# Kernel optimization log

Measured on AMD Instinct MI355X. Metric: run time of the kernel, lower is better.

Reference implementation:

```python
import jax, jax.numpy as jnp
import numpy as np

B = 65536
NUM_INPUTS = 256
NUM_HIDDEN = 256


def setup_inputs() -> dict:
    key = jax.random.key(0)
    ks = jax.random.split(key, 11)
    f32 = jnp.float32
    return {
        "x": jax.random.normal(ks[0], (B, NUM_INPUTS), dtype=f32),
        "h_t_1": jax.random.normal(ks[1], (B, NUM_HIDDEN), dtype=f32),
        "Wz": jax.random.normal(ks[2], (NUM_INPUTS, NUM_HIDDEN), dtype=f32),
        "Uz": jax.random.normal(ks[3], (NUM_HIDDEN, NUM_HIDDEN), dtype=f32),
        "bz": jax.random.normal(ks[4], (NUM_HIDDEN,), dtype=f32),
        "Wr": jax.random.normal(ks[5], (NUM_INPUTS, NUM_HIDDEN), dtype=f32),
        "Ur": jax.random.normal(ks[6], (NUM_HIDDEN, NUM_HIDDEN), dtype=f32),
        "br": jax.random.normal(ks[7], (NUM_HIDDEN,), dtype=f32),
        "Wh": jax.random.normal(ks[8], (NUM_INPUTS, NUM_HIDDEN), dtype=f32),
        "Uh": jax.random.normal(ks[9], (NUM_HIDDEN, NUM_HIDDEN), dtype=f32),
        "bh": jax.random.normal(ks[10], (NUM_HIDDEN,), dtype=f32),
    }


def reference(x, h_t_1, Wz, Uz, bz, Wr, Ur, br, Wh, Uh, bh):
    # update gate z = sigmoid(x@Wz + h@Uz + bz)
    z = jax.nn.sigmoid(x @ Wz + h_t_1 @ Uz + bz)
    # reset gate r = sigmoid(x@Wr + h@Ur + br)
    r = jax.nn.sigmoid(x @ Wr + h_t_1 @ Ur + br)
    # candidate: tanh(x@Wh + (r*h)@Uh + bh)
    h_hat = jnp.tanh(x @ Wh + (r * h_t_1) @ Uh + bh)
    h_t = z * h_t_1 + (1.0 - z) * h_hat
    return (h_t, h_t)
```

## Files before the change

### kernel.cpp

```cpp
#include <hip/hip_runtime.h>
#include <hip/hip_fp16.h>


#define NHID 256
#define B_ROWS 65536
#define MT 32
#define RT 2
#define CPW 4
#define GATE_STRIDE (16 * 16 * 64 * 8)

typedef _Float16 half8 __attribute__((ext_vector_type(8)));
typedef _Float16 half4_t __attribute__((ext_vector_type(4)));
typedef _Float16 half2_t __attribute__((ext_vector_type(2)));
typedef float floatx4 __attribute__((ext_vector_type(4)));

__device__ __forceinline__ int lidx(int m, int c) {
    return m * 256 + ((((c >> 3) ^ (m & 7)) << 3)) + (c & 7);
}

__device__ __forceinline__ void barrier_lgkm() {
    __builtin_amdgcn_sched_barrier(0);
    asm volatile("s_waitcnt lgkmcnt(0)" ::: "memory");
    __builtin_amdgcn_s_barrier();
    __builtin_amdgcn_sched_barrier(0);
}

__global__ __launch_bounds__(256) void pack_weights_kernel(
    const float* __restrict__ Wz, const float* __restrict__ Uz,
    const float* __restrict__ Wr, const float* __restrict__ Ur,
    const float* __restrict__ Wh, const float* __restrict__ Uh,
    _Float16* __restrict__ packed)
{
    int tid = blockIdx.x * blockDim.x + threadIdx.x;
    int lane = tid & 63;
    int s    = (tid >> 6) & 15;
    int ct   = (tid >> 10) & 15;
    int g    = tid >> 14;
    const float* W = (g == 0) ? Wz : (g == 1) ? Wr : Wh;
    const float* U = (g == 0) ? Uz : (g == 1) ? Ur : Uh;
    int n  = ct * 16 + (lane & 15);
    int k0 = s * 32 + (lane >> 4) * 8;
    half8 v;
#pragma unroll
    for (int j = 0; j < 8; ++j) {
        int k = k0 + j;
        float f = (k < 256) ? W[k * 256 + n] : U[(k - 256) * 256 + n];
        v[j] = (_Float16)f;
    }
    *reinterpret_cast<half8*>(packed + (size_t)tid * 8) = v;
}

#define WFRAG(base, ct, s) \
    (*reinterpret_cast<const half8*>((base) + (size_t)((((ct) * 16 + (s)) * 64 + lane) * 8)))

__global__ __launch_bounds__(256, 2) void gru_main_kernel(
    const float* __restrict__ x, const float* __restrict__ h,
    const _Float16* __restrict__ wpack,
    const float* __restrict__ bz, const float* __restrict__ br,
    const float* __restrict__ bh,
    float* __restrict__ out)
{
    __shared__ __align__(16) _Float16 lsm[MT * 256 * 2];
    _Float16* lx = lsm;
    _Float16* lh = lsm + MT * 256;

    const int tid  = threadIdx.x;
    const int lane = tid & 63;
    const int wave = tid >> 6;
    const int row0 = blockIdx.x * MT;
    const int m_lo = lane & 15;
    const int quad = lane >> 4;
    const int mx   = m_lo & 7;
    const int ct0  = wave * CPW;

    const _Float16* wz = wpack;
    const _Float16* wr = wpack + GATE_STRIDE;
    const _Float16* wh = wpack + 2 * GATE_STRIDE;

    half8 wzb[2][2], wrb[2][2];
    wzb[0][0] = WFRAG(wz, ct0 + 0, 0);
    wzb[0][1] = WFRAG(wz, ct0 + 1, 0);
    wrb[0][0] = WFRAG(wr, ct0 + 0, 0);
    wrb[0][1] = WFRAG(wr, ct0 + 1, 0);

    {
        const float4* xv = reinterpret_cast<const float4*>(x + (size_t)row0 * NHID);
        const float4* hv = reinterpret_cast<const float4*>(h + (size_t)row0 * NHID);
#pragma unroll
        for (int it = 0; it < (MT * 64) / 256; ++it) {
            int i = it * 256 + tid;
            int m = i >> 6;
            int c = (i & 63) * 4;
            float4 a = xv[i];
            float4 b = hv[i];
            half4_t va = { (_Float16)a.x, (_Float16)a.y, (_Float16)a.z, (_Float16)a.w };
            half4_t vb = { (_Float16)b.x, (_Float16)b.y, (_Float16)b.z, (_Float16)b.w };
            *reinterpret_cast<half4_t*>(&lx[lidx(m, c)]) = va;
            *reinterpret_cast<half4_t*>(&lh[lidx(m, c)]) = vb;
        }
    }
    barrier_lgkm();

    half2_t zpk[CPW][RT][4];

    floatx4 accz[CPW][RT];
    floatx4 accr[CPW][RT];
#pragma unroll
    for (int c = 0; c < CPW; ++c)
#pragma unroll
        for (int rt = 0; rt < RT; ++rt) {
            accz[c][rt] = (floatx4){0.f, 0.f, 0.f, 0.f};
            accr[c][rt] = (floatx4){0.f, 0.f, 0.f, 0.f};
        }

#pragma unroll
    for (int s = 0; s < 16; ++s) {
        const _Float16* asrc = (s < 8) ? lx : lh;
        const int kcx = (((s & 7) * 4 + quad) ^ mx) << 3;
        half8 af[RT];
#pragma unroll
        for (int rt = 0; rt < RT; ++rt)
            af[rt] = *reinterpret_cast<const half8*>(&asrc[(rt * 16 + m_lo) * 256 + kcx]);
#pragma unroll
        for (int p = 0; p < 2; ++p) {
            const int u = s * 2 + p;
            if (u < 31) {
                const int ns = (p == 1) ? s + 1 : s;
                const int nc = ct0 + (p ^ 1) * 2;
                wzb[p ^ 1][0] = WFRAG(wz, nc + 0, ns);
                wzb[p ^ 1][1] = WFRAG(wz, nc + 1, ns);
                wrb[p ^ 1][0] = WFRAG(wr, nc + 0, ns);
                wrb[p ^ 1][1] = WFRAG(wr, nc + 1, ns);
            }
            __builtin_amdgcn_s_setprio(1);
#pragma unroll
            for (int q = 0; q < 2; ++q) {
                const int c = p * 2 + q;
#pragma unroll
                for (int rt = 0; rt < RT; ++rt) {
                    accz[c][rt] = __builtin_amdgcn_mfma_f32_16x16x32_f16(af[rt], wzb[p][q], accz[c][rt], 0, 0, 0);
                    accr[c][rt] = __builtin_amdgcn_mfma_f32_16x16x32_f16(af[rt], wrb[p][q], accr[c][rt], 0, 0, 0);
                }
            }
            __builtin_amdgcn_s_setprio(0);
        }
    }

    half8 whb[2][2];
    whb[0][0] = WFRAG(wh, ct0 + 0, 0);
    whb[0][1] = WFRAG(wh, ct0 + 1, 0);
    float bzv[CPW], brv[CPW], bhv[CPW];
#pragma unroll
    for (int c = 0; c < CPW; ++c) {
        const int col = (ct0 + c) * 16 + m_lo;
        bzv[c] = bz[col];
        brv[c] = br[col];
        bhv[c] = bh[col];
    }

    barrier_lgkm();

#pragma unroll
    for (int c = 0; c < CPW; ++c) {
        const int col = (ct0 + c) * 16 + m_lo;
#pragma unroll
        for (int rt = 0; rt < RT; ++rt) {
#pragma unroll
            for (int e = 0; e < 4; ++e) {
                const int row = rt * 16 + quad * 4 + e;
                float sz = accz[c][rt][e] + bzv[c];
                float sr = accr[c][rt][e] + brv[c];
                float zv = 1.f / (1.f + __expf(-sz));
                float rv = 1.f / (1.f + __expf(-sr));
                const int li = lidx(row, col);
                float hval = (float)lh[li];
                lh[li] = (_Float16)(rv * hval);
                zpk[c][rt][e] = half2_t{ (_Float16)(zv * hval), (_Float16)(1.f - zv) };
            }
        }
    }

    floatx4 acch[CPW][RT];
#pragma unroll
    for (int c = 0; c < CPW; ++c)
#pragma unroll
        for (int rt = 0; rt < RT; ++rt)
            acch[c][rt] = (floatx4){0.f, 0.f, 0.f, 0.f};

#pragma unroll
    for (int s = 0; s < 16; ++s) {
        if (s == 8) barrier_lgkm();
        const _Float16* asrc = (s < 8) ? lx : lh;
        const int kcx = (((s & 7) * 4 + quad) ^ mx) << 3;
        half8 af[RT];
#pragma unroll
        for (int rt = 0; rt < RT; ++rt)
            af[rt] = *reinterpret_cast<const half8*>(&asrc[(rt * 16 + m_lo) * 256 + kcx]);
#pragma unroll
        for (int p = 0; p < 2; ++p) {
            const int u = s * 2 + p;
            if (u < 31) {
                const int ns = (p == 1) ? s + 1 : s;
                const int nc = ct0 + (p ^ 1) * 2;
                whb[p ^ 1][0] = WFRAG(wh, nc + 0, ns);
                whb[p ^ 1][1] = WFRAG(wh, nc + 1, ns);
            }
            __builtin_amdgcn_s_setprio(1);
#pragma unroll
            for (int q = 0; q < 2; ++q) {
                const int c = p * 2 + q;
#pragma unroll
                for (int rt = 0; rt < RT; ++rt)
                    acch[c][rt] = __builtin_amdgcn_mfma_f32_16x16x32_f16(af[rt], whb[p][q], acch[c][rt], 0, 0, 0);
            }
            __builtin_amdgcn_s_setprio(0);
        }
    }

    const size_t OUT2 = (size_t)B_ROWS * NHID;
#pragma unroll
    for (int c = 0; c < CPW; ++c) {
        const int col = (ct0 + c) * 16 + m_lo;
#pragma unroll
        for (int rt = 0; rt < RT; ++rt) {
#pragma unroll
            for (int e = 0; e < 4; ++e) {
                const int row = rt * 16 + quad * 4 + e;
                float sh = acch[c][rt][e] + bhv[c];
                float e2 = __expf(2.f * sh);
                float hh = 1.f - 2.f / (e2 + 1.f);
                float zh  = (float)zpk[c][rt][e][0];
                float omz = (float)zpk[c][rt][e][1];
                float ht  = zh + omz * hh;
                size_t idx = (size_t)(row0 + row) * NHID + col;
                __builtin_nontemporal_store(ht, &out[idx]);
                __builtin_nontemporal_store(ht, &out[OUT2 + idx]);
            }
        }
    }
}

extern "C" void kernel_launch(void* const* d_in, const int* in_sizes, int n_in,
                              void* d_out, int out_size, void* d_ws, size_t ws_size,
                              hipStream_t stream) {
    (void)in_sizes; (void)n_in; (void)out_size; (void)ws_size;
    const float* x  = (const float*)d_in[0];
    const float* h  = (const float*)d_in[1];
    const float* Wz = (const float*)d_in[2];
    const float* Uz = (const float*)d_in[3];
    const float* bz = (const float*)d_in[4];
    const float* Wr = (const float*)d_in[5];
    const float* Ur = (const float*)d_in[6];
    const float* br = (const float*)d_in[7];
    const float* Wh = (const float*)d_in[8];
    const float* Uh = (const float*)d_in[9];
    const float* bh = (const float*)d_in[10];
    float* out = (float*)d_out;
    _Float16* wpack = (_Float16*)d_ws;

    pack_weights_kernel<<<192, 256, 0, stream>>>(Wz, Uz, Wr, Ur, Wh, Uh, wpack);
    gru_main_kernel<<<B_ROWS / MT, 256, 0, stream>>>(x, h, wpack, bz, br, bh, out);
}
```

Measured before the change: 312.4 us.

## Process two row tiles per block with next-tile input prefetch overlapped

```diff
diff --git a/kernel.cpp b/kernel.cpp
--- a/kernel.cpp
+++ b/kernel.cpp
@@ -7,6 +7,7 @@
 #define MT 32
 #define RT 2
 #define CPW 4
+#define NBLK 1024
 #define GATE_STRIDE (16 * 16 * 64 * 8)
 
 typedef _Float16 half8 __attribute__((ext_vector_type(8)));
@@ -67,88 +68,24 @@
     const int tid  = threadIdx.x;
     const int lane = tid & 63;
     const int wave = tid >> 6;
-    const int row0 = blockIdx.x * MT;
     const int m_lo = lane & 15;
     const int quad = lane >> 4;
     const int mx   = m_lo & 7;
     const int ct0  = wave * CPW;
+    const int sc   = (tid & 63) * 4;
 
     const _Float16* wz = wpack;
     const _Float16* wr = wpack + GATE_STRIDE;
     const _Float16* wh = wpack + 2 * GATE_STRIDE;
-
-    half8 wzb[2][2], wrb[2][2];
-    wzb[0][0] = WFRAG(wz, ct0 + 0, 0);
-    wzb[0][1] = WFRAG(wz, ct0 + 1, 0);
-    wrb[0][0] = WFRAG(wr, ct0 + 0, 0);
-    wrb[0][1] = WFRAG(wr, ct0 + 1, 0);
-
-    {
-        const float4* xv = reinterpret_cast<const float4*>(x + (size_t)row0 * NHID);
-        const float4* hv = reinterpret_cast<const float4*>(h + (size_t)row0 * NHID);
-#pragma unroll
-        for (int it = 0; it < (MT * 64) / 256; ++it) {
-            int i = it * 256 + tid;
-            int m = i >> 6;
-            int c = (i & 63) * 4;
-            float4 a = xv[i];
-            float4 b = hv[i];
-            half4_t va = { (_Float16)a.x, (_Float16)a.y, (_Float16)a.z, (_Float16)a.w };
-            half4_t vb = { (_Float16)b.x, (_Float16)b.y, (_Float16)b.z, (_Float16)b.w };
-            *reinterpret_cast<half4_t*>(&lx[lidx(m, c)]) = va;
-            *reinterpret_cast<half4_t*>(&lh[lidx(m, c)]) = vb;
-        }
-    }
-    barrier_lgkm();
-
-    half2_t zpk[CPW][RT][4];
-
-    floatx4 accz[CPW][RT];
-    floatx4 accr[CPW][RT];
-#pragma unroll
-    for (int c = 0; c < CPW; ++c)
-#pragma unroll
-        for (int rt = 0; rt < RT; ++rt) {
-            accz[c][rt] = (floatx4){0.f, 0.f, 0.f, 0.f};
-            accr[c][rt] = (floatx4){0.f, 0.f, 0.f, 0.f};
-        }
-
-#pragma unroll
-    for (int s = 0; s < 16; ++s) {
-        const _Float16* asrc = (s < 8) ? lx : lh;
-        const int kcx = (((s & 7) * 4 + quad) ^ mx) << 3;
-        half8 af[RT];
-#pragma unroll
-        for (int rt = 0; rt < RT; ++rt)
-            af[rt] = *reinterpret_cast<const half8*>(&asrc[(rt * 16 + m_lo) * 256 + kcx]);
-#pragma unroll
-        for (int p = 0; p < 2; ++p) {
-            const int u = s * 2 + p;
-            if (u < 31) {
-                const int ns = (p == 1) ? s + 1 : s;
-                const int nc = ct0 + (p ^ 1) * 2;
-                wzb[p ^ 1][0] = WFRAG(wz, nc + 0, ns);
-                wzb[p ^ 1][1] = WFRAG(wz, nc + 1, ns);
-                wrb[p ^ 1][0] = WFRAG(wr, nc + 0, ns);
-                wrb[p ^ 1][1] = WFRAG(wr, nc + 1, ns);
-            }
-            __builtin_amdgcn_s_setprio(1);
-#pragma unroll
-            for (int q = 0; q < 2; ++q) {
-                const int c = p * 2 + q;
-#pragma unroll
-                for (int rt = 0; rt < RT; ++rt) {
-                    accz[c][rt] = __builtin_amdgcn_mfma_f32_16x16x32_f16(af[rt], wzb[p][q], accz[c][rt], 0, 0, 0);
-                    accr[c][rt] = __builtin_amdgcn_mfma_f32_16x16x32_f16(af[rt], wrb[p][q], accr[c][rt], 0, 0, 0);
-                }
-            }
-            __builtin_amdgcn_s_setprio(0);
-        }
-    }
-
-    half8 whb[2][2];
-    whb[0][0] = WFRAG(wh, ct0 + 0, 0);
-    whb[0][1] = WFRAG(wh, ct0 + 1, 0);
+    const float4* xv4 = reinterpret_cast<const float4*>(x);
+    const float4* hv4 = reinterpret_cast<const float4*>(h);
+
+    auto stage_wr = [&](_Float16* dst, const float4& v, int it) {
+        const int m = it * 4 + wave;
+        half4_t p = { (_Float16)v.x, (_Float16)v.y, (_Float16)v.z, (_Float16)v.w };
+        *reinterpret_cast<half4_t*>(&dst[lidx(m, sc)]) = p;
+    };
+
     float bzv[CPW], brv[CPW], bhv[CPW];
 #pragma unroll
     for (int c = 0; c < CPW; ++c) {
@@ -158,84 +95,193 @@
         bhv[c] = bh[col];
     }
 
+    half8 wzb[2][2], wrb[2][2];
+    wzb[0][0] = WFRAG(wz, ct0 + 0, 0);
+    wzb[0][1] = WFRAG(wz, ct0 + 1, 0);
+    wrb[0][0] = WFRAG(wr, ct0 + 0, 0);
+    wrb[0][1] = WFRAG(wr, ct0 + 1, 0);
+
+    {
+        const size_t ib = (size_t)(blockIdx.x * MT) * 64 + tid;
+#pragma unroll
+        for (int it = 0; it < 8; ++it) {
+            float4 a = xv4[ib + it * 256];
+            float4 b = hv4[ib + it * 256];
+            stage_wr(lx, a, it);
+            stage_wr(lh, b, it);
+        }
+    }
     barrier_lgkm();
 
-#pragma unroll
-    for (int c = 0; c < CPW; ++c) {
-        const int col = (ct0 + c) * 16 + m_lo;
-#pragma unroll
-        for (int rt = 0; rt < RT; ++rt) {
-#pragma unroll
-            for (int e = 0; e < 4; ++e) {
-                const int row = rt * 16 + quad * 4 + e;
-                float sz = accz[c][rt][e] + bzv[c];
-                float sr = accr[c][rt][e] + brv[c];
-                float zv = 1.f / (1.f + __expf(-sz));
-                float rv = 1.f / (1.f + __expf(-sr));
-                const int li = lidx(row, col);
-                float hval = (float)lh[li];
-                lh[li] = (_Float16)(rv * hval);
-                zpk[c][rt][e] = half2_t{ (_Float16)(zv * hval), (_Float16)(1.f - zv) };
-            }
-        }
-    }
-
-    floatx4 acch[CPW][RT];
-#pragma unroll
-    for (int c = 0; c < CPW; ++c)
-#pragma unroll
-        for (int rt = 0; rt < RT; ++rt)
-            acch[c][rt] = (floatx4){0.f, 0.f, 0.f, 0.f};
-
-#pragma unroll
-    for (int s = 0; s < 16; ++s) {
-        if (s == 8) barrier_lgkm();
-        const _Float16* asrc = (s < 8) ? lx : lh;
-        const int kcx = (((s & 7) * 4 + quad) ^ mx) << 3;
-        half8 af[RT];
-#pragma unroll
-        for (int rt = 0; rt < RT; ++rt)
-            af[rt] = *reinterpret_cast<const half8*>(&asrc[(rt * 16 + m_lo) * 256 + kcx]);
-#pragma unroll
-        for (int p = 0; p < 2; ++p) {
-            const int u = s * 2 + p;
-            if (u < 31) {
-                const int ns = (p == 1) ? s + 1 : s;
-                const int nc = ct0 + (p ^ 1) * 2;
-                whb[p ^ 1][0] = WFRAG(wh, nc + 0, ns);
-                whb[p ^ 1][1] = WFRAG(wh, nc + 1, ns);
-            }
-            __builtin_amdgcn_s_setprio(1);
-#pragma unroll
-            for (int q = 0; q < 2; ++q) {
-                const int c = p * 2 + q;
-#pragma unroll
-                for (int rt = 0; rt < RT; ++rt)
-                    acch[c][rt] = __builtin_amdgcn_mfma_f32_16x16x32_f16(af[rt], whb[p][q], acch[c][rt], 0, 0, 0);
-            }
-            __builtin_amdgcn_s_setprio(0);
-        }
-    }
-
     const size_t OUT2 = (size_t)B_ROWS * NHID;
-#pragma unroll
-    for (int c = 0; c < CPW; ++c) {
-        const int col = (ct0 + c) * 16 + m_lo;
-#pragma unroll
-        for (int rt = 0; rt < RT; ++rt) {
-#pragma unroll
-            for (int e = 0; e < 4; ++e) {
-                const int row = rt * 16 + quad * 4 + e;
-                float sh = acch[c][rt][e] + bhv[c];
-                float e2 = __expf(2.f * sh);
-                float hh = 1.f - 2.f / (e2 + 1.f);
-                float zh  = (float)zpk[c][rt][e][0];
-                float omz = (float)zpk[c][rt][e][1];
-                float ht  = zh + omz * hh;
-                size_t idx = (size_t)(row0 + row) * NHID + col;
-                __builtin_nontemporal_store(ht, &out[idx]);
-                __builtin_nontemporal_store(ht, &out[OUT2 + idx]);
-            }
+
+#pragma unroll
+    for (int tile = 0; tile < 2; ++tile) {
+        const int row0   = (blockIdx.x + tile * NBLK) * MT;
+        const size_t nib = (size_t)((blockIdx.x + NBLK) * MT) * 64 + tid;
+
+        half2_t zpk[CPW][RT][4];
+
+        floatx4 accz[CPW][RT];
+        floatx4 accr[CPW][RT];
+#pragma unroll
+        for (int c = 0; c < CPW; ++c)
+#pragma unroll
+            for (int rt = 0; rt < RT; ++rt) {
+                accz[c][rt] = (floatx4){0.f, 0.f, 0.f, 0.f};
+                accr[c][rt] = (floatx4){0.f, 0.f, 0.f, 0.f};
+            }
+
+#pragma unroll
+        for (int s = 0; s < 16; ++s) {
+            if (tile == 1 && s == 8) barrier_lgkm();
+            const _Float16* asrc = (s < 8) ? lx : lh;
+            const int kcx = (((s & 7) * 4 + quad) ^ mx) << 3;
+            half8 af[RT];
+#pragma unroll
+            for (int rt = 0; rt < RT; ++rt)
+                af[rt] = *reinterpret_cast<const half8*>(&asrc[(rt * 16 + m_lo) * 256 + kcx]);
+#pragma unroll
+            for (int p = 0; p < 2; ++p) {
+                const int u = s * 2 + p;
+                if (u < 31) {
+                    const int ns = (p == 1) ? s + 1 : s;
+                    const int nc = ct0 + (p ^ 1) * 2;
+                    wzb[p ^ 1][0] = WFRAG(wz, nc + 0, ns);
+                    wzb[p ^ 1][1] = WFRAG(wz, nc + 1, ns);
+                    wrb[p ^ 1][0] = WFRAG(wr, nc + 0, ns);
+                    wrb[p ^ 1][1] = WFRAG(wr, nc + 1, ns);
+                }
+                __builtin_amdgcn_s_setprio(1);
+#pragma unroll
+                for (int q = 0; q < 2; ++q) {
+                    const int c = p * 2 + q;
+#pragma unroll
+                    for (int rt = 0; rt < RT; ++rt) {
+                        accz[c][rt] = __builtin_amdgcn_mfma_f32_16x16x32_f16(af[rt], wzb[p][q], accz[c][rt], 0, 0, 0);
+                        accr[c][rt] = __builtin_amdgcn_mfma_f32_16x16x32_f16(af[rt], wrb[p][q], accr[c][rt], 0, 0, 0);
+                    }
+                }
+                __builtin_amdgcn_s_setprio(0);
+            }
+        }
+
+        half8 whb[2][2];
+        whb[0][0] = WFRAG(wh, ct0 + 0, 0);
+        whb[0][1] = WFRAG(wh, ct0 + 1, 0);
+
+        barrier_lgkm();
+
+#pragma unroll
+        for (int c = 0; c < CPW; ++c) {
+#pragma unroll
+            for (int rt = 0; rt < RT; ++rt) {
+#pragma unroll
+                for (int e = 0; e < 4; ++e) {
+                    const int row = rt * 16 + quad * 4 + e;
+                    const int col = (ct0 + c) * 16 + m_lo;
+                    float sz = accz[c][rt][e] + bzv[c];
+                    float sr = accr[c][rt][e] + brv[c];
+                    float zv = 1.f / (1.f + __expf(-sz));
+                    float rv = 1.f / (1.f + __expf(-sr));
+                    const int li = lidx(row, col);
+                    float hval = (float)lh[li];
+                    lh[li] = (_Float16)(rv * hval);
+                    zpk[c][rt][e] = half2_t{ (_Float16)(zv * hval), (_Float16)(1.f - zv) };
+                }
+            }
+        }
+
+        floatx4 acch[CPW][RT];
+#pragma unroll
+        for (int c = 0; c < CPW; ++c)
+#pragma unroll
+            for (int rt = 0; rt < RT; ++rt)
+                acch[c][rt] = (floatx4){0.f, 0.f, 0.f, 0.f};
+
+        float4 xra[4], xrb[4], hr[8];
+
+#pragma unroll
+        for (int s = 0; s < 16; ++s) {
+            if (s == 8) {
+                barrier_lgkm();
+                if (tile == 0) {
+#pragma unroll
+                    for (int it = 0; it < 4; ++it)
+                        xra[it] = xv4[nib + it * 256];
+                }
+            }
+            if (s == 12 && tile == 0) {
+#pragma unroll
+                for (int it = 0; it < 4; ++it) stage_wr(lx, xra[it], it);
+#pragma unroll
+                for (int it = 0; it < 4; ++it)
+                    xrb[it] = xv4[nib + (it + 4) * 256];
+            }
+            const _Float16* asrc = (s < 8) ? lx : lh;
+            const int kcx = (((s & 7) * 4 + quad) ^ mx) << 3;
+            half8 af[RT];
+#pragma unroll
+            for (int rt = 0; rt < RT; ++rt)
+                af[rt] = *reinterpret_cast<const half8*>(&asrc[(rt * 16 + m_lo) * 256 + kcx]);
+#pragma unroll
+            for (int p = 0; p < 2; ++p) {
+                const int u = s * 2 + p;
+                if (u < 31) {
+                    const int ns = (p == 1) ? s + 1 : s;
+                    const int nc = ct0 + (p ^ 1) * 2;
+                    whb[p ^ 1][0] = WFRAG(wh, nc + 0, ns);
+                    whb[p ^ 1][1] = WFRAG(wh, nc + 1, ns);
+                }
+                __builtin_amdgcn_s_setprio(1);
+#pragma unroll
+                for (int q = 0; q < 2; ++q) {
+                    const int c = p * 2 + q;
+#pragma unroll
+                    for (int rt = 0; rt < RT; ++rt)
+                        acch[c][rt] = __builtin_amdgcn_mfma_f32_16x16x32_f16(af[rt], whb[p][q], acch[c][rt], 0, 0, 0);
+                }
+                __builtin_amdgcn_s_setprio(0);
+            }
+        }
+
+        if (tile == 0) {
+#pragma unroll
+            for (int it = 0; it < 4; ++it) stage_wr(lx, xrb[it], it + 4);
+#pragma unroll
+            for (int it = 0; it < 8; ++it) hr[it] = hv4[nib + it * 256];
+            wzb[0][0] = WFRAG(wz, ct0 + 0, 0);
+            wzb[0][1] = WFRAG(wz, ct0 + 1, 0);
+            wrb[0][0] = WFRAG(wr, ct0 + 0, 0);
+            wrb[0][1] = WFRAG(wr, ct0 + 1, 0);
+        }
+
+        barrier_lgkm();
+
+#pragma unroll
+        for (int c = 0; c < CPW; ++c) {
+            const int col = (ct0 + c) * 16 + m_lo;
+#pragma unroll
+            for (int rt = 0; rt < RT; ++rt) {
+#pragma unroll
+                for (int e = 0; e < 4; ++e) {
+                    const int row = rt * 16 + quad * 4 + e;
+                    float sh = acch[c][rt][e] + bhv[c];
+                    float e2 = __expf(2.f * sh);
+                    float hh = 1.f - 2.f / (e2 + 1.f);
+                    float zh  = (float)zpk[c][rt][e][0];
+                    float omz = (float)zpk[c][rt][e][1];
+                    float ht  = zh + omz * hh;
+                    size_t idx = (size_t)(row0 + row) * NHID + col;
+                    out[idx] = ht;
+                    out[OUT2 + idx] = ht;
+                }
+            }
+        }
+
+        if (tile == 0) {
+#pragma unroll
+            for (int it = 0; it < 8; ++it) stage_wr(lh, hr[it], it);
         }
     }
 }
@@ -259,5 +305,5 @@
     _Float16* wpack = (_Float16*)d_ws;
 
     pack_weights_kernel<<<192, 256, 0, stream>>>(Wz, Uz, Wr, Ur, Wh, Uh, wpack);
-    gru_main_kernel<<<B_ROWS / MT, 256, 0, stream>>>(x, h, wpack, bz, br, bh, out);
-}
+    gru_main_kernel<<<NBLK, 256, 0, stream>>>(x, h, wpack, bz, br, bh, out);
+}
```

Result: no change. 314.4 us (+0.6%).

## Make blocks loop over four row tiles with double-buffered LDS prefetch

Applied to the files above, without the earlier changes.

```diff
diff --git a/kernel.cpp b/kernel.cpp
--- a/kernel.cpp
+++ b/kernel.cpp
@@ -7,6 +7,9 @@
 #define MT 32
 #define RT 2
 #define CPW 4
+#define TPB 4
+#define NBLK 512
+#define TILEH (MT * 256)
 #define GATE_STRIDE (16 * 16 * 64 * 8)
 
 typedef _Float16 half8 __attribute__((ext_vector_type(8)));
@@ -60,22 +63,38 @@
     const float* __restrict__ bh,
     float* __restrict__ out)
 {
-    __shared__ __align__(16) _Float16 lsm[MT * 256 * 2];
-    _Float16* lx = lsm;
-    _Float16* lh = lsm + MT * 256;
-
-    const int tid  = threadIdx.x;
-    const int lane = tid & 63;
-    const int wave = tid >> 6;
-    const int row0 = blockIdx.x * MT;
-    const int m_lo = lane & 15;
-    const int quad = lane >> 4;
-    const int mx   = m_lo & 7;
-    const int ct0  = wave * CPW;
+    __shared__ __align__(16) _Float16 lsm[4 * TILEH];
+
+    const int tid   = threadIdx.x;
+    const int lane  = tid & 63;
+    const int wave  = tid >> 6;
+    const int m_lo  = lane & 15;
+    const int quad  = lane >> 4;
+    const int mx    = m_lo & 7;
+    const int ct0   = wave * CPW;
+    const int lane4 = lane * 4;
 
     const _Float16* wz = wpack;
     const _Float16* wr = wpack + GATE_STRIDE;
     const _Float16* wh = wpack + 2 * GATE_STRIDE;
+    const float4* xv4 = reinterpret_cast<const float4*>(x);
+    const float4* hv4 = reinterpret_cast<const float4*>(h);
+    const size_t OUT2 = (size_t)B_ROWS * NHID;
+
+    auto stage_wr = [&](_Float16* dst, const float4& v, int j) {
+        const int m = j * 4 + wave;
+        half4_t p = { (_Float16)v.x, (_Float16)v.y, (_Float16)v.z, (_Float16)v.w };
+        *reinterpret_cast<half4_t*>(&dst[lidx(m, lane4)]) = p;
+    };
+
+    float bzv[CPW], brv[CPW], bhv[CPW];
+#pragma unroll
+    for (int c = 0; c < CPW; ++c) {
+        const int col = (ct0 + c) * 16 + m_lo;
+        bzv[c] = bz[col];
+        brv[c] = br[col];
+        bhv[c] = bh[col];
+    }
 
     half8 wzb[2][2], wrb[2][2];
     wzb[0][0] = WFRAG(wz, ct0 + 0, 0);
@@ -84,157 +103,171 @@
     wrb[0][1] = WFRAG(wr, ct0 + 1, 0);
 
     {
-        const float4* xv = reinterpret_cast<const float4*>(x + (size_t)row0 * NHID);
-        const float4* hv = reinterpret_cast<const float4*>(h + (size_t)row0 * NHID);
-#pragma unroll
-        for (int it = 0; it < (MT * 64) / 256; ++it) {
-            int i = it * 256 + tid;
-            int m = i >> 6;
-            int c = (i & 63) * 4;
-            float4 a = xv[i];
-            float4 b = hv[i];
-            half4_t va = { (_Float16)a.x, (_Float16)a.y, (_Float16)a.z, (_Float16)a.w };
-            half4_t vb = { (_Float16)b.x, (_Float16)b.y, (_Float16)b.z, (_Float16)b.w };
-            *reinterpret_cast<half4_t*>(&lx[lidx(m, c)]) = va;
-            *reinterpret_cast<half4_t*>(&lh[lidx(m, c)]) = vb;
+        const size_t ib = (size_t)(blockIdx.x * TPB * MT) * 64 + tid;
+#pragma unroll
+        for (int j = 0; j < 8; ++j) {
+            float4 a = xv4[ib + j * 256];
+            float4 b = hv4[ib + j * 256];
+            stage_wr(lsm, a, j);
+            stage_wr(lsm + TILEH, b, j);
         }
     }
     barrier_lgkm();
 
-    half2_t zpk[CPW][RT][4];
-
-    floatx4 accz[CPW][RT];
-    floatx4 accr[CPW][RT];
-#pragma unroll
-    for (int c = 0; c < CPW; ++c)
-#pragma unroll
-        for (int rt = 0; rt < RT; ++rt) {
-            accz[c][rt] = (floatx4){0.f, 0.f, 0.f, 0.f};
-            accr[c][rt] = (floatx4){0.f, 0.f, 0.f, 0.f};
-        }
-
-#pragma unroll
-    for (int s = 0; s < 16; ++s) {
-        const _Float16* asrc = (s < 8) ? lx : lh;
-        const int kcx = (((s & 7) * 4 + quad) ^ mx) << 3;
-        half8 af[RT];
-#pragma unroll
-        for (int rt = 0; rt < RT; ++rt)
-            af[rt] = *reinterpret_cast<const half8*>(&asrc[(rt * 16 + m_lo) * 256 + kcx]);
-#pragma unroll
-        for (int p = 0; p < 2; ++p) {
-            const int u = s * 2 + p;
-            if (u < 31) {
-                const int ns = (p == 1) ? s + 1 : s;
-                const int nc = ct0 + (p ^ 1) * 2;
-                wzb[p ^ 1][0] = WFRAG(wz, nc + 0, ns);
-                wzb[p ^ 1][1] = WFRAG(wz, nc + 1, ns);
-                wrb[p ^ 1][0] = WFRAG(wr, nc + 0, ns);
-                wrb[p ^ 1][1] = WFRAG(wr, nc + 1, ns);
-            }
-            __builtin_amdgcn_s_setprio(1);
-#pragma unroll
-            for (int q = 0; q < 2; ++q) {
-                const int c = p * 2 + q;
-#pragma unroll
-                for (int rt = 0; rt < RT; ++rt) {
-                    accz[c][rt] = __builtin_amdgcn_mfma_f32_16x16x32_f16(af[rt], wzb[p][q], accz[c][rt], 0, 0, 0);
-                    accr[c][rt] = __builtin_amdgcn_mfma_f32_16x16x32_f16(af[rt], wrb[p][q], accr[c][rt], 0, 0, 0);
-                }
-            }
-            __builtin_amdgcn_s_setprio(0);
-        }
-    }
-
-    half8 whb[2][2];
-    whb[0][0] = WFRAG(wh, ct0 + 0, 0);
-    whb[0][1] = WFRAG(wh, ct0 + 1, 0);
-    float bzv[CPW], brv[CPW], bhv[CPW];
-#pragma unroll
-    for (int c = 0; c < CPW; ++c) {
-        const int col = (ct0 + c) * 16 + m_lo;
-        bzv[c] = bz[col];
-        brv[c] = br[col];
-        bhv[c] = bh[col];
-    }
-
-    barrier_lgkm();
-
-#pragma unroll
-    for (int c = 0; c < CPW; ++c) {
-        const int col = (ct0 + c) * 16 + m_lo;
-#pragma unroll
-        for (int rt = 0; rt < RT; ++rt) {
-#pragma unroll
-            for (int e = 0; e < 4; ++e) {
-                const int row = rt * 16 + quad * 4 + e;
-                float sz = accz[c][rt][e] + bzv[c];
-                float sr = accr[c][rt][e] + brv[c];
-                float zv = 1.f / (1.f + __expf(-sz));
-                float rv = 1.f / (1.f + __expf(-sr));
-                const int li = lidx(row, col);
-                float hval = (float)lh[li];
-                lh[li] = (_Float16)(rv * hval);
-                zpk[c][rt][e] = half2_t{ (_Float16)(zv * hval), (_Float16)(1.f - zv) };
-            }
-        }
-    }
-
-    floatx4 acch[CPW][RT];
-#pragma unroll
-    for (int c = 0; c < CPW; ++c)
-#pragma unroll
-        for (int rt = 0; rt < RT; ++rt)
-            acch[c][rt] = (floatx4){0.f, 0.f, 0.f, 0.f};
-
-#pragma unroll
-    for (int s = 0; s < 16; ++s) {
-        if (s == 8) barrier_lgkm();
-        const _Float16* asrc = (s < 8) ? lx : lh;
-        const int kcx = (((s & 7) * 4 + quad) ^ mx) << 3;
-        half8 af[RT];
-#pragma unroll
-        for (int rt = 0; rt < RT; ++rt)
-            af[rt] = *reinterpret_cast<const half8*>(&asrc[(rt * 16 + m_lo) * 256 + kcx]);
-#pragma unroll
-        for (int p = 0; p < 2; ++p) {
-            const int u = s * 2 + p;
-            if (u < 31) {
-                const int ns = (p == 1) ? s + 1 : s;
-                const int nc = ct0 + (p ^ 1) * 2;
-                whb[p ^ 1][0] = WFRAG(wh, nc + 0, ns);
-                whb[p ^ 1][1] = WFRAG(wh, nc + 1, ns);
-            }
-            __builtin_amdgcn_s_setprio(1);
-#pragma unroll
-            for (int q = 0; q < 2; ++q) {
-                const int c = p * 2 + q;
-#pragma unroll
-                for (int rt = 0; rt < RT; ++rt)
-                    acch[c][rt] = __builtin_amdgcn_mfma_f32_16x16x32_f16(af[rt], whb[p][q], acch[c][rt], 0, 0, 0);
-            }
-            __builtin_amdgcn_s_setprio(0);
-        }
-    }
-
-    const size_t OUT2 = (size_t)B_ROWS * NHID;
-#pragma unroll
-    for (int c = 0; c < CPW; ++c) {
-        const int col = (ct0 + c) * 16 + m_lo;
-#pragma unroll
-        for (int rt = 0; rt < RT; ++rt) {
-#pragma unroll
-            for (int e = 0; e < 4; ++e) {
-                const int row = rt * 16 + quad * 4 + e;
-                float sh = acch[c][rt][e] + bhv[c];
-                float e2 = __expf(2.f * sh);
-                float hh = 1.f - 2.f / (e2 + 1.f);
-                float zh  = (float)zpk[c][rt][e][0];
-                float omz = (float)zpk[c][rt][e][1];
-                float ht  = zh + omz * hh;
-                size_t idx = (size_t)(row0 + row) * NHID + col;
-                __builtin_nontemporal_store(ht, &out[idx]);
-                __builtin_nontemporal_store(ht, &out[OUT2 + idx]);
+#pragma unroll 1
+    for (int t = 0; t < TPB; ++t) {
+        const int buf = t & 1;
+        _Float16* lxc = lsm + buf * (2 * TILEH);
+        _Float16* lhc = lxc + TILEH;
+        _Float16* lxn = lsm + (buf ^ 1) * (2 * TILEH);
+        _Float16* lhn = lxn + TILEH;
+        const int row0 = (blockIdx.x * TPB + t) * MT;
+        const size_t nib = (size_t)(row0 + MT) * 64 + tid;
+        const bool more = (t < TPB - 1);
+
+        half2_t zpk[CPW][RT][4];
+
+        floatx4 accz[CPW][RT];
+        floatx4 accr[CPW][RT];
+#pragma unroll
+        for (int c = 0; c < CPW; ++c)
+#pragma unroll
+            for (int rt = 0; rt < RT; ++rt) {
+                accz[c][rt] = (floatx4){0.f, 0.f, 0.f, 0.f};
+                accr[c][rt] = (floatx4){0.f, 0.f, 0.f, 0.f};
+            }
+
+        float4 xin;
+#pragma unroll
+        for (int s = 0; s < 16; ++s) {
+            if (more) {
+                if ((s & 1) == 0) xin = xv4[nib + (s >> 1) * 256];
+                else              stage_wr(lxn, xin, s >> 1);
+            }
+            const _Float16* asrc = (s < 8) ? lxc : lhc;
+            const int kcx = (((s & 7) * 4 + quad) ^ mx) << 3;
+            half8 af[RT];
+#pragma unroll
+            for (int rt = 0; rt < RT; ++rt)
+                af[rt] = *reinterpret_cast<const half8*>(&asrc[(rt * 16 + m_lo) * 256 + kcx]);
+#pragma unroll
+            for (int p = 0; p < 2; ++p) {
+                const int u = s * 2 + p;
+                if (u < 31) {
+                    const int ns = (p == 1) ? s + 1 : s;
+                    const int nc = ct0 + (p ^ 1) * 2;
+                    wzb[p ^ 1][0] = WFRAG(wz, nc + 0, ns);
+                    wzb[p ^ 1][1] = WFRAG(wz, nc + 1, ns);
+                    wrb[p ^ 1][0] = WFRAG(wr, nc + 0, ns);
+                    wrb[p ^ 1][1] = WFRAG(wr, nc + 1, ns);
+                }
+                __builtin_amdgcn_s_setprio(1);
+#pragma unroll
+                for (int q = 0; q < 2; ++q) {
+                    const int c = p * 2 + q;
+#pragma unroll
+                    for (int rt = 0; rt < RT; ++rt) {
+                        accz[c][rt] = __builtin_amdgcn_mfma_f32_16x16x32_f16(af[rt], wzb[p][q], accz[c][rt], 0, 0, 0);
+                        accr[c][rt] = __builtin_amdgcn_mfma_f32_16x16x32_f16(af[rt], wrb[p][q], accr[c][rt], 0, 0, 0);
+                    }
+                }
+                __builtin_amdgcn_s_setprio(0);
+            }
+        }
+
+        half8 whb[2][2];
+        whb[0][0] = WFRAG(wh, ct0 + 0, 0);
+        whb[0][1] = WFRAG(wh, ct0 + 1, 0);
+
+        barrier_lgkm();
+
+#pragma unroll
+        for (int c = 0; c < CPW; ++c) {
+            const int col = (ct0 + c) * 16 + m_lo;
+#pragma unroll
+            for (int rt = 0; rt < RT; ++rt) {
+#pragma unroll
+                for (int e = 0; e < 4; ++e) {
+                    const int row = rt * 16 + quad * 4 + e;
+                    float sz = accz[c][rt][e] + bzv[c];
+                    float sr = accr[c][rt][e] + brv[c];
+                    float zv = 1.f / (1.f + __expf(-sz));
+                    float rv = 1.f / (1.f + __expf(-sr));
+                    const int li = lidx(row, col);
+                    float hval = (float)lhc[li];
+                    lhc[li] = (_Float16)(rv * hval);
+                    zpk[c][rt][e] = half2_t{ (_Float16)(zv * hval), (_Float16)(1.f - zv) };
+                }
+            }
+        }
+
+        floatx4 acch[CPW][RT];
+#pragma unroll
+        for (int c = 0; c < CPW; ++c)
+#pragma unroll
+            for (int rt = 0; rt < RT; ++rt)
+                acch[c][rt] = (floatx4){0.f, 0.f, 0.f, 0.f};
+
+        float4 hin[2];
+#pragma unroll
+        for (int s = 0; s < 16; ++s) {
+            if (more) {
+                if (s >= 1 && s <= 8) stage_wr(lhn, hin[(s - 1) & 1], s - 1);
+                if (s < 8) hin[s & 1] = hv4[nib + s * 256];
+            }
+            if (s == 8) barrier_lgkm();
+            const _Float16* asrc = (s < 8) ? lxc : lhc;
+            const int kcx = (((s & 7) * 4 + quad) ^ mx) << 3;
+            half8 af[RT];
+#pragma unroll
+            for (int rt = 0; rt < RT; ++rt)
+                af[rt] = *reinterpret_cast<const half8*>(&asrc[(rt * 16 + m_lo) * 256 + kcx]);
+#pragma unroll
+            for (int p = 0; p < 2; ++p) {
+                const int u = s * 2 + p;
+                if (u < 31) {
+                    const int ns = (p == 1) ? s + 1 : s;
+                    const int nc = ct0 + (p ^ 1) * 2;
+                    whb[p ^ 1][0] = WFRAG(wh, nc + 0, ns);
+                    whb[p ^ 1][1] = WFRAG(wh, nc + 1, ns);
+                }
+                __builtin_amdgcn_s_setprio(1);
+#pragma unroll
+                for (int q = 0; q < 2; ++q) {
+                    const int c = p * 2 + q;
+#pragma unroll
+                    for (int rt = 0; rt < RT; ++rt)
+                        acch[c][rt] = __builtin_amdgcn_mfma_f32_16x16x32_f16(af[rt], whb[p][q], acch[c][rt], 0, 0, 0);
+                }
+                __builtin_amdgcn_s_setprio(0);
+            }
+        }
+
+        if (more) {
+            wzb[0][0] = WFRAG(wz, ct0 + 0, 0);
+            wzb[0][1] = WFRAG(wz, ct0 + 1, 0);
+            wrb[0][0] = WFRAG(wr, ct0 + 0, 0);
+            wrb[0][1] = WFRAG(wr, ct0 + 1, 0);
+        }
+
+#pragma unroll
+        for (int c = 0; c < CPW; ++c) {
+            const int col = (ct0 + c) * 16 + m_lo;
+#pragma unroll
+            for (int rt = 0; rt < RT; ++rt) {
+#pragma unroll
+                for (int e = 0; e < 4; ++e) {
+                    const int row = rt * 16 + quad * 4 + e;
+                    float sh = acch[c][rt][e] + bhv[c];
+                    float e2 = __expf(2.f * sh);
+                    float hh = 1.f - 2.f / (e2 + 1.f);
+                    float zh  = (float)zpk[c][rt][e][0];
+                    float omz = (float)zpk[c][rt][e][1];
+                    float ht  = zh + omz * hh;
+                    size_t idx = (size_t)(row0 + row) * NHID + col;
+                    __builtin_nontemporal_store(ht, &out[idx]);
+                    __builtin_nontemporal_store(ht, &out[OUT2 + idx]);
+                }
             }
         }
     }
@@ -259,5 +292,5 @@
     _Float16* wpack = (_Float16*)d_ws;
 
     pack_weights_kernel<<<192, 256, 0, stream>>>(Wz, Uz, Wr, Ur, Wh, Uh, wpack);
-    gru_main_kernel<<<B_ROWS / MT, 256, 0, stream>>>(x, h, wpack, bz, br, bh, out);
-}
+    gru_main_kernel<<<NBLK, 256, 0, stream>>>(x, h, wpack, bz, br, bh, out);
+}
```

New measurement: 734.6 us. +135.1%, slower.
